# Performance work log

Measured on AMD Instinct MI355X. Metric: run time of the kernel, lower is better.

## Reference

```python
import jax, jax.numpy as jnp
import numpy as np

EPS = 1e-5
NUM_GRAPHS = 512


def _glorot(key, shape):
    lim = float(np.sqrt(6.0 / (shape[0] + shape[1])))
    return jax.random.uniform(key, shape, jnp.float32, -lim, lim)


def setup_inputs() -> dict:
    key = jax.random.key(0)
    ks = jax.random.split(key, 20)
    N, E, F0 = 50000, 800000, 64
    x = jax.random.normal(ks[0], (N, F0), jnp.float32)
    edge_index = jax.random.randint(ks[1], (2, E), 0, N, jnp.int64)
    batch = jnp.sort(jax.random.randint(ks[2], (N,), 0, NUM_GRAPHS, jnp.int64))
    dims = [(F0, 128), (128, 64), (64, 32)]
    p = {}
    for i, (di, do) in enumerate(dims, start=1):
        p[f"W{i}l"] = _glorot(ks[3 * i], (di, do))
        p[f"b{i}"] = jnp.zeros((do,), jnp.float32)
        p[f"W{i}r"] = _glorot(ks[3 * i + 1], (di, do))
        p[f"g{i}"] = jnp.ones((do,), jnp.float32)
        p[f"be{i}"] = jnp.zeros((do,), jnp.float32)
    p["Wf1"] = _glorot(ks[13], (32, 128)); p["bf1"] = jnp.zeros((128,), jnp.float32)
    p["Wf2"] = _glorot(ks[14], (128, 64)); p["bf2"] = jnp.zeros((64,), jnp.float32)
    p["Wf3"] = _glorot(ks[15], (64, 2)); p["bf3"] = jnp.zeros((2,), jnp.float32)
    return {"x": x, "edge_index": edge_index, "batch": batch, **p}


def _sage(x, src, dst, Wl, bl, Wr, n):
    # mean-aggregate neighbor features (gather from src, scatter-mean to dst)
    agg = jax.ops.segment_sum(x[src], dst, num_segments=n)
    cnt = jax.ops.segment_sum(jnp.ones((src.shape[0],), x.dtype), dst, num_segments=n)
    mean = agg / jnp.maximum(cnt, 1.0)[:, None]
    return mean @ Wl + bl + x @ Wr


def _bn(x, g, b):
    mu = jnp.mean(x, axis=0)
    var = jnp.mean((x - mu) ** 2, axis=0)  # biased var, torch training mode
    return (x - mu) * jax.lax.rsqrt(var + EPS) * g + b


def reference(x, edge_index, batch,
              W1l, b1, W1r, g1, be1,
              W2l, b2, W2r, g2, be2,
              W3l, b3, W3r, g3, be3,
              Wf1, bf1, Wf2, bf2, Wf3, bf3):
    n = x.shape[0]
    src, dst = edge_index[0], edge_index[1]
    h = _bn(jax.nn.relu(_sage(x, src, dst, W1l, b1, W1r, n)), g1, be1)
    h = _bn(jax.nn.relu(_sage(h, src, dst, W2l, b2, W2r, n)), g2, be2)
    h = _bn(jax.nn.relu(_sage(h, src, dst, W3l, b3, W3r, n)), g3, be3)
    pooled = jax.ops.segment_sum(h, batch, num_segments=NUM_GRAPHS)  # [G, 32]
    cr = jax.nn.relu(pooled @ Wf1 + bf1)  # dropout = identity (eval)
    cr = jax.nn.relu(cr @ Wf2 + bf2)
    cr = cr @ Wf3 + bf3
    return cr.reshape(-1, 2)
```

## Files before the change

kernel.cpp:

```cpp
#include <hip/hip_runtime.h>
#include <hip/hip_bf16.h>

#define EPSBN 1e-5f
#define NGRAPH 512
#define SCAN_NB 128

typedef __attribute__((ext_vector_type(8))) short bf16x8;
typedef __attribute__((ext_vector_type(4))) float f32x4;

__device__ inline short f2bf(float f) {
    unsigned u = __builtin_bit_cast(unsigned, f);
    u += 0x7fffu + ((u >> 16) & 1u);
    return (short)(u >> 16);
}
__device__ inline float bf2f(short s) {
    unsigned u = ((unsigned)(unsigned short)s) << 16;
    return __builtin_bit_cast(float, u);
}

__global__ void __launch_bounds__(256) k_hist(
    const int* __restrict__ dst, int* __restrict__ hist, int E)
{
    for (int e = blockIdx.x * 256 + threadIdx.x; e < E; e += gridDim.x * 256)
        atomicAdd(&hist[dst[e]], 1);
}

__global__ void __launch_bounds__(256) k_scan1(
    const int* __restrict__ hist, int* __restrict__ blocksum, int N)
{
    __shared__ int red[256];
    const int C = (N + SCAN_NB - 1) / SCAN_NB;
    const int b = blockIdx.x, t = threadIdx.x;
    const int lo = b * C, hi = min(lo + C, N);
    int s = 0;
    for (int i = lo + t; i < hi; i += 256) s += hist[i];
    red[t] = s;
    __syncthreads();
    for (int off = 128; off; off >>= 1) {
        if (t < off) red[t] += red[t + off];
        __syncthreads();
    }
    if (t == 0) blocksum[b] = red[0];
}

__global__ void __launch_bounds__(SCAN_NB) k_scan2(
    const int* __restrict__ blocksum, int* __restrict__ blockoff,
    int* __restrict__ row_off, int N)
{
    __shared__ int tmp[SCAN_NB];
    const int t = threadIdx.x;
    int v = blocksum[t];
    tmp[t] = v;
    __syncthreads();
    for (int off = 1; off < SCAN_NB; off <<= 1) {
        int u = (t >= off) ? tmp[t - off] : 0;
        __syncthreads();
        tmp[t] += u;
        __syncthreads();
    }
    blockoff[t] = tmp[t] - v;
    if (t == SCAN_NB - 1) row_off[N] = tmp[t];
}

__global__ void __launch_bounds__(256) k_scan3(
    const int* __restrict__ hist, const int* __restrict__ blockoff,
    int* __restrict__ row_off, int* __restrict__ cursor, int N)
{
    __shared__ int red[256];
    const int C = (N + SCAN_NB - 1) / SCAN_NB;
    const int b = blockIdx.x, t = threadIdx.x;
    const int lo = b * C, hi = min(lo + C, N);
    const int TC = (C + 255) / 256;
    const int s0 = lo + t * TC;
    const int s1 = min(s0 + TC, hi);
    int s = 0;
    for (int i = s0; i < s1; i++) s += hist[i];
    red[t] = s;
    __syncthreads();
    for (int off = 1; off < 256; off <<= 1) {
        int u = (t >= off) ? red[t - off] : 0;
        __syncthreads();
        red[t] += u;
        __syncthreads();
    }
    int run = blockoff[b] + red[t] - s;
    for (int i = s0; i < s1; i++) {
        row_off[i] = run;
        cursor[i] = run;
        run += hist[i];
    }
}

__global__ void __launch_bounds__(256) k_scatter(
    const int* __restrict__ src, const int* __restrict__ dst,
    int* __restrict__ cursor, int* __restrict__ csr, int E)
{
    for (int e = blockIdx.x * 256 + threadIdx.x; e < E; e += gridDim.x * 256) {
        int d = dst[e];
        int p = atomicAdd(&cursor[d], 1);
        csr[p] = src[e];
    }
}

template <int F, bool OB>
__global__ void __launch_bounds__(256) k_gatherb(
    const short* __restrict__ feat, const int* __restrict__ row_off,
    const int* __restrict__ csr, void* __restrict__ aggv, int N)
{
    constexpr int LPR = F / 8;
    constexpr int RPB = 256 / LPR;
    const int lane = threadIdx.x % LPR;
    const int rloc = threadIdx.x / LPR;
    float* aggf = (float*)aggv;
    short* aggb = (short*)aggv;
    for (int row = blockIdx.x * RPB + rloc; row < N; row += gridDim.x * RPB) {
        const int s0 = row_off[row];
        const int s1 = row_off[row + 1];
        float acc0[8], acc1[8];
        #pragma unroll
        for (int i = 0; i < 8; i++) { acc0[i] = 0.f; acc1[i] = 0.f; }
        int p = s0;
        for (; p + 1 < s1; p += 2) {
            int sA = csr[p];
            int sB = csr[p + 1];
            bf16x8 va = *(const bf16x8*)&feat[(long long)sA * F + lane * 8];
            bf16x8 vb = *(const bf16x8*)&feat[(long long)sB * F + lane * 8];
            #pragma unroll
            for (int i = 0; i < 8; i++) {
                acc0[i] += bf2f(va[i]);
                acc1[i] += bf2f(vb[i]);
            }
        }
        if (p < s1) {
            int sA = csr[p];
            bf16x8 va = *(const bf16x8*)&feat[(long long)sA * F + lane * 8];
            #pragma unroll
            for (int i = 0; i < 8; i++) acc0[i] += bf2f(va[i]);
        }
        if constexpr (OB) {
            short o[8];
            #pragma unroll
            for (int i = 0; i < 8; i++) o[i] = f2bf(acc0[i] + acc1[i]);
            *(bf16x8*)&aggb[(long long)row * F + lane * 8] = *(bf16x8*)o;
        } else {
            float4 o0 = make_float4(acc0[0] + acc1[0], acc0[1] + acc1[1],
                                    acc0[2] + acc1[2], acc0[3] + acc1[3]);
            float4 o1 = make_float4(acc0[4] + acc1[4], acc0[5] + acc1[5],
                                    acc0[6] + acc1[6], acc0[7] + acc1[7]);
            *(float4*)&aggf[(long long)row * F + lane * 8] = o0;
            *(float4*)&aggf[(long long)row * F + lane * 8 + 4] = o1;
        }
    }
}

__global__ void __launch_bounds__(256) k_cvt(
    const float* __restrict__ in, short* __restrict__ out, long long n4)
{
    long long i = (long long)blockIdx.x * 256 + threadIdx.x;
    if (i >= n4) return;
    float4 v = *(const float4*)&in[i * 4];
    short4 o = make_short4(f2bf(v.x), f2bf(v.y), f2bf(v.z), f2bf(v.w));
    *(short4*)&out[i * 4] = o;
}

template <int K, int F, bool AFF>
__global__ void __launch_bounds__(64) k_wprep(
    const float* __restrict__ W, const float* __restrict__ a,
    const float* __restrict__ c, const float* __restrict__ bias,
    short* __restrict__ Wt, float* __restrict__ cvec)
{
    int j = blockIdx.x * 64 + threadIdx.x;
    if (j >= F) return;
    float cv = bias ? bias[j] : 0.f;
    for (int k = 0; k < K; k++) {
        float w = W[k * F + j];
        float aa = 1.f;
        if constexpr (AFF) {
            aa = a[k];
            cv += c[k] * w;
        }
        Wt[j * K + k] = f2bf(aa * w);
    }
    cvec[j] = cv;
}

template <int K, int FOUT, bool DUAL, bool HASBASE, bool FINAL, bool OUTBF16>
__global__ void __launch_bounds__(256) k_mgemm(
    const short* __restrict__ A, const short* __restrict__ A2,
    const short* __restrict__ Wt, const short* __restrict__ Wt2,
    const float* __restrict__ cvec, const float* __restrict__ base,
    const int* __restrict__ row_off, void* outv,
    float* __restrict__ s_out, float* __restrict__ q_out, int N)
{
    constexpr int KS = K / 32;
    constexpr int NCT = FOUT / 16;
    const int lane = threadIdx.x & 63;
    const int wid = threadIdx.x >> 6;
    const int g = lane >> 4;
    const int mi = lane & 15;
    const int RT = (N + 15) >> 4;
    const int nw = gridDim.x * 4;
    float* outf = (float*)outv;
    short* outb = (short*)outv;

    float st_s[FINAL ? NCT : 1];
    float st_q[FINAL ? NCT : 1];
    if constexpr (FINAL) {
        #pragma unroll
        for (int ct = 0; ct < NCT; ct++) { st_s[ct] = 0.f; st_q[ct] = 0.f; }
    }

    for (int rt = blockIdx.x * 4 + wid; rt < RT; rt += nw) {
        const int m0 = rt * 16;
        int arow = m0 + mi;
        if (arow >= N) arow = N - 1;

        bf16x8 af[KS];
        bf16x8 af2[DUAL ? KS : 1];
        const short* ap = A + (long long)arow * K;
        #pragma unroll
        for (int s = 0; s < KS; s++)
            af[s] = *(const bf16x8*)(ap + s * 32 + g * 8);
        if constexpr (DUAL) {
            const short* ap2 = A2 + (long long)arow * K;
            #pragma unroll
            for (int s = 0; s < KS; s++)
                af2[s] = *(const bf16x8*)(ap2 + s * 32 + g * 8);
        }

        float invc[4];
        if constexpr (DUAL || HASBASE) {
            #pragma unroll
            for (int r = 0; r < 4; r++) {
                int row = m0 + 4 * g + r;
                int cnt = 1;
                if (row < N) cnt = max(row_off[row + 1] - row_off[row], 1);
                invc[r] = 1.f / (float)cnt;
            }
        }

        #pragma unroll
        for (int ct = 0; ct < NCT; ct++) {
            f32x4 acc = {0.f, 0.f, 0.f, 0.f};
            f32x4 acc2 = {0.f, 0.f, 0.f, 0.f};
            const short* bp = Wt + (long long)(ct * 16 + mi) * K;
            #pragma unroll
            for (int s = 0; s < KS; s++) {
                bf16x8 bf = *(const bf16x8*)(bp + s * 32 + g * 8);
                acc = __builtin_amdgcn_mfma_f32_16x16x32_bf16(af[s], bf, acc, 0, 0, 0);
                if constexpr (DUAL) {
                    bf16x8 bf2 = *(const bf16x8*)(Wt2 + (long long)(ct * 16 + mi) * K + s * 32 + g * 8);
                    acc2 = __builtin_amdgcn_mfma_f32_16x16x32_bf16(af2[s], bf2, acc2, 0, 0, 0);
                }
            }
            float cv = cvec[ct * 16 + mi];
            float sl = 0.f, ql = 0.f;
            #pragma unroll
            for (int r = 0; r < 4; r++) {
                int row = m0 + 4 * g + r;
                if (row < N) {
                    float v = acc[r] + cv;
                    if constexpr (DUAL) v = fmaf(invc[r], acc2[r], v);
                    if constexpr (HASBASE)
                        v = fmaf(invc[r], base[(long long)row * FOUT + ct * 16 + mi], v);
                    if constexpr (FINAL) v = fmaxf(v, 0.f);
                    if constexpr (OUTBF16)
                        outb[(long long)row * FOUT + ct * 16 + mi] = f2bf(v);
                    else
                        outf[(long long)row * FOUT + ct * 16 + mi] = v;
                    if constexpr (FINAL) { sl += v; ql += v * v; }
                }
            }
            if constexpr (FINAL) {
                sl += __shfl_xor(sl, 16, 64);
                sl += __shfl_xor(sl, 32, 64);
                ql += __shfl_xor(ql, 16, 64);
                ql += __shfl_xor(ql, 32, 64);
                st_s[ct] += sl;
                st_q[ct] += ql;
            }
        }
    }

    if constexpr (FINAL) {
        __shared__ float redS[4][NCT][16];
        __shared__ float redQ[4][NCT][16];
        if (lane < 16) {
            #pragma unroll
            for (int ct = 0; ct < NCT; ct++) {
                redS[wid][ct][lane] = st_s[ct];
                redQ[wid][ct][lane] = st_q[ct];
            }
        }
        __syncthreads();
        if (wid == 0 && lane < 16) {
            #pragma unroll
            for (int ct = 0; ct < NCT; ct++) {
                float s = redS[0][ct][lane] + redS[1][ct][lane] +
                          redS[2][ct][lane] + redS[3][ct][lane];
                float q = redQ[0][ct][lane] + redQ[1][ct][lane] +
                          redQ[2][ct][lane] + redQ[3][ct][lane];
                atomicAdd(&s_out[ct * 16 + lane], s);
                atomicAdd(&q_out[ct * 16 + lane], q);
            }
        }
    }
}

__global__ void k_finalize(const float* __restrict__ s, const float* __restrict__ q,
                           const float* __restrict__ g, const float* __restrict__ be,
                           float* __restrict__ a, float* __restrict__ c,
                           int F, float invN)
{
    int j = threadIdx.x;
    if (j < F) {
        float mu = s[j] * invN;
        float var = q[j] * invN - mu * mu;
        float aj = g[j] / sqrtf(var + EPSBN);
        a[j] = aj;
        c[j] = be[j] - mu * aj;
    }
}

__global__ void __launch_bounds__(256) k_pool(
    const float* __restrict__ t3, const float* __restrict__ a,
    const float* __restrict__ c, const int* __restrict__ batch,
    float* __restrict__ pooled, int N)
{
    long long gid = (long long)blockIdx.x * 256 + threadIdx.x;
    int i = (int)(gid >> 5);
    int j = (int)(gid & 31);
    if (i >= N) return;
    int g = batch[i];
    float v = t3[(long long)i * 32 + j] * a[j] + c[j];
    atomicAdd(&pooled[g * 32 + j], v);
}

__global__ void __launch_bounds__(128) k_mlp(
    const float* __restrict__ pooled,
    const float* __restrict__ Wf1, const float* __restrict__ bf1,
    const float* __restrict__ Wf2, const float* __restrict__ bf2,
    const float* __restrict__ Wf3, const float* __restrict__ bf3,
    float* __restrict__ out)
{
    __shared__ float p[32], h1[128], h2[64];
    int g = blockIdx.x, t = threadIdx.x;
    if (t < 32) p[t] = pooled[g * 32 + t];
    __syncthreads();
    {
        float acc = bf1[t];
        #pragma unroll
        for (int k = 0; k < 32; k++) acc += p[k] * Wf1[k * 128 + t];
        h1[t] = fmaxf(acc, 0.f);
    }
    __syncthreads();
    if (t < 64) {
        float acc = bf2[t];
        #pragma unroll
        for (int k = 0; k < 128; k++) acc += h1[k] * Wf2[k * 64 + t];
        h2[t] = fmaxf(acc, 0.f);
    }
    __syncthreads();
    if (t < 2) {
        float acc = bf3[t];
        #pragma unroll
        for (int k = 0; k < 64; k++) acc += h2[k] * Wf3[k * 2 + t];
        out[g * 2 + t] = acc;
    }
}

extern "C" void kernel_launch(void* const* d_in, const int* in_sizes, int n_in,
                              void* d_out, int out_size, void* d_ws, size_t ws_size,
                              hipStream_t stream)
{
    const float* x     = (const float*)d_in[0];
    const int*   ei    = (const int*)d_in[1];
    const int*   batch = (const int*)d_in[2];
    const float* W1l = (const float*)d_in[3];
    const float* b1  = (const float*)d_in[4];
    const float* W1r = (const float*)d_in[5];
    const float* g1  = (const float*)d_in[6];
    const float* be1 = (const float*)d_in[7];
    const float* W2l = (const float*)d_in[8];
    const float* b2  = (const float*)d_in[9];
    const float* W2r = (const float*)d_in[10];
    const float* g2  = (const float*)d_in[11];
    const float* be2 = (const float*)d_in[12];
    const float* W3l = (const float*)d_in[13];
    const float* b3  = (const float*)d_in[14];
    const float* W3r = (const float*)d_in[15];
    const float* g3  = (const float*)d_in[16];
    const float* be3 = (const float*)d_in[17];
    const float* Wf1 = (const float*)d_in[18];
    const float* bf1 = (const float*)d_in[19];
    const float* Wf2 = (const float*)d_in[20];
    const float* bf2 = (const float*)d_in[21];
    const float* Wf3 = (const float*)d_in[22];
    const float* bf3 = (const float*)d_in[23];

    const int N = in_sizes[0] / 64;
    const int E = in_sizes[1] / 2;
    const int* src = ei;
    const int* dst = ei + E;

    char* ws = (char*)d_ws;
    size_t off = 0;
    auto alloc = [&](size_t bytes) {
        size_t o = off;
        off += (bytes + 511) & ~(size_t)511;
        return o;
    };
    const size_t o_rowoff = alloc((size_t)(N + 1) * 4);
    const size_t o_hist   = alloc((size_t)N * 4);
    const size_t o_cursor = alloc((size_t)N * 4);
    const size_t o_bsum   = alloc(SCAN_NB * 4 * 2);
    const size_t o_csr    = alloc((size_t)E * 4);
    const size_t o_zoneB  = alloc((size_t)N * 128);
    const size_t o_zoneC  = alloc((size_t)N * 128);
    const size_t o_zoneD  = alloc((size_t)N * 256);
    const size_t o_zoneE  = alloc((size_t)N * 256);
    const size_t o_pool   = alloc((size_t)NGRAPH * 32 * 4);
    const size_t o_stats  = alloc(448 * 4);
    const size_t o_aff    = alloc(448 * 4);
    const size_t o_cvec   = alloc(512 * 4);
    const size_t o_wt     = alloc((8192 * 4 + 2048 * 2) * 2);
    (void)ws_size;

    int* row_off = (int*)(ws + o_rowoff);
    int* hist    = (int*)(ws + o_hist);
    int* cursor  = (int*)(ws + o_cursor);
    int* bsum    = (int*)(ws + o_bsum);
    int* boff    = bsum + SCAN_NB;
    int* csr     = (int*)(ws + o_csr);
    short* xb   = (short*)(ws + o_zoneB);
    short* y2b  = (short*)(ws + o_zoneB);
    short* aggb = (short*)(ws + o_zoneC);
    short* t2b  = (short*)(ws + o_zoneC);
    short* t1b  = (short*)(ws + o_zoneD);
    short* y3b  = (short*)(ws + o_zoneD);
    float* m2   = (float*)(ws + o_zoneE);
    float* m3   = (float*)(ws + o_zoneE);
    float* t3   = m3;
    float* pooled = (float*)(ws + o_pool);
    float* s1 = (float*)(ws + o_stats);
    float* q1 = s1 + 128;
    float* s2 = q1 + 128;
    float* q2 = s2 + 64;
    float* s3 = q2 + 64;
    float* q3 = s3 + 32;
    float* a1 = (float*)(ws + o_aff);
    float* c1 = a1 + 128;
    float* a2 = c1 + 128;
    float* c2 = a2 + 64;
    float* a3 = c2 + 64;
    float* c3 = a3 + 32;
    float* cv1r = (float*)(ws + o_cvec);
    float* cvdum = cv1r + 128;
    float* cv2l = cvdum + 128;
    float* cv2r = cv2l + 64;
    float* cv3l = cv2r + 64;
    float* cv3r = cv3l + 32;
    short* W1l_t = (short*)(ws + o_wt);
    short* W1r_t = W1l_t + 8192;
    short* W2l_t = W1r_t + 8192;
    short* W2r_t = W2l_t + 8192;
    short* W3l_t = W2r_t + 8192;
    short* W3r_t = W3l_t + 2048;

    const float invN = 1.0f / (float)N;
    const int MG = 512;

    hipMemsetAsync(ws + o_hist, 0, (size_t)N * 4, stream);
    hipMemsetAsync(ws + o_stats, 0, 448 * 4, stream);
    hipMemsetAsync(ws + o_pool, 0, (size_t)NGRAPH * 32 * 4, stream);

    k_hist<<<2048, 256, 0, stream>>>(dst, hist, E);
    k_scan1<<<SCAN_NB, 256, 0, stream>>>(hist, bsum, N);
    k_scan2<<<1, SCAN_NB, 0, stream>>>(bsum, boff, row_off, N);
    k_scan3<<<SCAN_NB, 256, 0, stream>>>(hist, boff, row_off, cursor, N);
    k_scatter<<<2048, 256, 0, stream>>>(src, dst, cursor, csr, E);

    k_cvt<<<(int)(((long long)N * 16 + 255) / 256), 256, 0, stream>>>(
        x, xb, (long long)N * 16);
    k_wprep<64, 128, false><<<2, 64, 0, stream>>>(
        W1r, nullptr, nullptr, b1, W1r_t, cv1r);
    k_wprep<64, 128, false><<<2, 64, 0, stream>>>(
        W1l, nullptr, nullptr, nullptr, W1l_t, cvdum);

    k_gatherb<64, true><<<(N + 31) / 32, 256, 0, stream>>>(
        xb, row_off, csr, aggb, N);
    k_mgemm<64, 128, true, false, true, true><<<MG, 256, 0, stream>>>(
        xb, aggb, W1r_t, W1l_t, cv1r, nullptr, row_off, t1b, s1, q1, N);
    k_finalize<<<1, 128, 0, stream>>>(s1, q1, g1, be1, a1, c1, 128, invN);

    k_wprep<128, 64, true><<<1, 64, 0, stream>>>(W2l, a1, c1, nullptr, W2l_t, cv2l);
    k_wprep<128, 64, true><<<1, 64, 0, stream>>>(W2r, a1, c1, b2, W2r_t, cv2r);
    k_mgemm<128, 64, false, false, false, true><<<MG, 256, 0, stream>>>(
        t1b, nullptr, W2l_t, nullptr, cv2l, nullptr, row_off, y2b,
        nullptr, nullptr, N);
    k_gatherb<64, false><<<(N + 31) / 32, 256, 0, stream>>>(
        y2b, row_off, csr, m2, N);
    k_mgemm<128, 64, false, true, true, true><<<MG, 256, 0, stream>>>(
        t1b, nullptr, W2r_t, nullptr, cv2r, m2, row_off, t2b, s2, q2, N);
    k_finalize<<<1, 64, 0, stream>>>(s2, q2, g2, be2, a2, c2, 64, invN);

    k_wprep<64, 32, true><<<1, 64, 0, stream>>>(W3l, a2, c2, nullptr, W3l_t, cv3l);
    k_wprep<64, 32, true><<<1, 64, 0, stream>>>(W3r, a2, c2, b3, W3r_t, cv3r);
    k_mgemm<64, 32, false, false, false, true><<<MG, 256, 0, stream>>>(
        t2b, nullptr, W3l_t, nullptr, cv3l, nullptr, row_off, y3b,
        nullptr, nullptr, N);
    k_gatherb<32, false><<<(N + 63) / 64, 256, 0, stream>>>(
        y3b, row_off, csr, m3, N);
    k_mgemm<64, 32, false, true, true, false><<<MG, 256, 0, stream>>>(
        t2b, nullptr, W3r_t, nullptr, cv3r, m3, row_off, t3, s3, q3, N);
    k_finalize<<<1, 32, 0, stream>>>(s3, q3, g3, be3, a3, c3, 32, invN);

    {
        long long tot = (long long)N * 32;
        int blocks = (int)((tot + 255) / 256);
        k_pool<<<blocks, 256, 0, stream>>>(t3, a3, c3, batch, pooled, N);
    }
    k_mlp<<<NGRAPH, 128, 0, stream>>>(pooled, Wf1, bf1, Wf2, bf2, Wf3, bf3,
                                      (float*)d_out);
}
```

Before: 312.4 us.

## Partition CSR scatter by XCD, store aggregates in bf16, fuse pooling into final GEMM

The CSR scatter kernel now has each block handle only destinations in one eighth of the node range, chosen by blockIdx mod 8, to keep cursor atomics local to one XCD's cache. The layer-2 and layer-3 neighbor aggregates are now stored in bf16 instead of fp32, which halves their traffic. The separate pooling kernel is removed: the last GEMM atomically adds its raw ReLU outputs into per-graph sums, and the BN affine is applied afterwards in the MLP using per-graph node counts. In exchange, every block reads all edges in the scatter, bf16 storage of the aggregates loses precision, and the GEMM epilogue now does many atomics on a small array.

```diff
diff --git a/kernel.cpp b/kernel.cpp
--- a/kernel.cpp
+++ b/kernel.cpp
@@ -4,6 +4,7 @@
 #define EPSBN 1e-5f
 #define NGRAPH 512
 #define SCAN_NB 128
+#define NXCD 8
 
 typedef __attribute__((ext_vector_type(8))) short bf16x8;
 typedef __attribute__((ext_vector_type(4))) float f32x4;
@@ -91,28 +92,33 @@
     }
 }
 
-__global__ void __launch_bounds__(256) k_scatter(
+__global__ void __launch_bounds__(256) k_scatter8(
     const int* __restrict__ src, const int* __restrict__ dst,
-    int* __restrict__ cursor, int* __restrict__ csr, int E)
-{
-    for (int e = blockIdx.x * 256 + threadIdx.x; e < E; e += gridDim.x * 256) {
+    int* __restrict__ cursor, int* __restrict__ csr, int E, int N)
+{
+    const int grp = blockIdx.x & (NXCD - 1);
+    const int chunk = (N + NXCD - 1) / NXCD;
+    const int lo = grp * chunk;
+    const int hi = min(lo + chunk, N);
+    const int stride = (gridDim.x >> 3) * 256;
+    for (int e = (blockIdx.x >> 3) * 256 + threadIdx.x; e < E; e += stride) {
         int d = dst[e];
-        int p = atomicAdd(&cursor[d], 1);
-        csr[p] = src[e];
-    }
-}
-
-template <int F, bool OB>
+        if (d >= lo && d < hi) {
+            int p = atomicAdd(&cursor[d], 1);
+            csr[p] = src[e];
+        }
+    }
+}
+
+template <int F>
 __global__ void __launch_bounds__(256) k_gatherb(
     const short* __restrict__ feat, const int* __restrict__ row_off,
-    const int* __restrict__ csr, void* __restrict__ aggv, int N)
+    const int* __restrict__ csr, short* __restrict__ aggb, int N)
 {
     constexpr int LPR = F / 8;
     constexpr int RPB = 256 / LPR;
     const int lane = threadIdx.x % LPR;
     const int rloc = threadIdx.x / LPR;
-    float* aggf = (float*)aggv;
-    short* aggb = (short*)aggv;
     for (int row = blockIdx.x * RPB + rloc; row < N; row += gridDim.x * RPB) {
         const int s0 = row_off[row];
         const int s1 = row_off[row + 1];
@@ -137,19 +143,10 @@
             #pragma unroll
             for (int i = 0; i < 8; i++) acc0[i] += bf2f(va[i]);
         }
-        if constexpr (OB) {
-            short o[8];
-            #pragma unroll
-            for (int i = 0; i < 8; i++) o[i] = f2bf(acc0[i] + acc1[i]);
-            *(bf16x8*)&aggb[(long long)row * F + lane * 8] = *(bf16x8*)o;
-        } else {
-            float4 o0 = make_float4(acc0[0] + acc1[0], acc0[1] + acc1[1],
-                                    acc0[2] + acc1[2], acc0[3] + acc1[3]);
-            float4 o1 = make_float4(acc0[4] + acc1[4], acc0[5] + acc1[5],
-                                    acc0[6] + acc1[6], acc0[7] + acc1[7]);
-            *(float4*)&aggf[(long long)row * F + lane * 8] = o0;
-            *(float4*)&aggf[(long long)row * F + lane * 8 + 4] = o1;
-        }
+        short o[8];
+        #pragma unroll
+        for (int i = 0; i < 8; i++) o[i] = f2bf(acc0[i] + acc1[i]);
+        *(bf16x8*)&aggb[(long long)row * F + lane * 8] = *(bf16x8*)o;
     }
 }
 
@@ -184,13 +181,15 @@
     cvec[j] = cv;
 }
 
-template <int K, int FOUT, bool DUAL, bool HASBASE, bool FINAL, bool OUTBF16>
+template <int K, int FOUT, bool DUAL, bool HASBASE, bool FINAL, bool OUTBF16,
+          bool POOL>
 __global__ void __launch_bounds__(256) k_mgemm(
     const short* __restrict__ A, const short* __restrict__ A2,
     const short* __restrict__ Wt, const short* __restrict__ Wt2,
-    const float* __restrict__ cvec, const float* __restrict__ base,
+    const float* __restrict__ cvec, const short* __restrict__ base,
     const int* __restrict__ row_off, void* outv,
-    float* __restrict__ s_out, float* __restrict__ q_out, int N)
+    float* __restrict__ s_out, float* __restrict__ q_out,
+    const int* __restrict__ batchp, float* __restrict__ praw, int N)
 {
     constexpr int KS = K / 32;
     constexpr int NCT = FOUT / 16;
@@ -238,6 +237,14 @@
                 invc[r] = 1.f / (float)cnt;
             }
         }
+        int bidx[4];
+        if constexpr (POOL) {
+            #pragma unroll
+            for (int r = 0; r < 4; r++) {
+                int row = m0 + 4 * g + r;
+                bidx[r] = (row < N) ? batchp[row] : -1;
+            }
+        }
 
         #pragma unroll
         for (int ct = 0; ct < NCT; ct++) {
@@ -262,12 +269,15 @@
                     float v = acc[r] + cv;
                     if constexpr (DUAL) v = fmaf(invc[r], acc2[r], v);
                     if constexpr (HASBASE)
-                        v = fmaf(invc[r], base[(long long)row * FOUT + ct * 16 + mi], v);
+                        v = fmaf(invc[r], bf2f(base[(long long)row * FOUT + ct * 16 + mi]), v);
                     if constexpr (FINAL) v = fmaxf(v, 0.f);
-                    if constexpr (OUTBF16)
+                    if constexpr (POOL) {
+                        atomicAdd(&praw[bidx[r] * FOUT + ct * 16 + mi], v);
+                    } else if constexpr (OUTBF16) {
                         outb[(long long)row * FOUT + ct * 16 + mi] = f2bf(v);
-                    else
+                    } else {
                         outf[(long long)row * FOUT + ct * 16 + mi] = v;
+                    }
                     if constexpr (FINAL) { sl += v; ql += v * v; }
                 }
             }
@@ -322,22 +332,16 @@
     }
 }
 
-__global__ void __launch_bounds__(256) k_pool(
-    const float* __restrict__ t3, const float* __restrict__ a,
-    const float* __restrict__ c, const int* __restrict__ batch,
-    float* __restrict__ pooled, int N)
-{
-    long long gid = (long long)blockIdx.x * 256 + threadIdx.x;
-    int i = (int)(gid >> 5);
-    int j = (int)(gid & 31);
-    if (i >= N) return;
-    int g = batch[i];
-    float v = t3[(long long)i * 32 + j] * a[j] + c[j];
-    atomicAdd(&pooled[g * 32 + j], v);
+__global__ void __launch_bounds__(256) k_gcnt(
+    const int* __restrict__ batch, float* __restrict__ gcnt, int N)
+{
+    int i = blockIdx.x * 256 + threadIdx.x;
+    if (i < N) atomicAdd(&gcnt[batch[i]], 1.0f);
 }
 
 __global__ void __launch_bounds__(128) k_mlp(
-    const float* __restrict__ pooled,
+    const float* __restrict__ praw, const float* __restrict__ a3,
+    const float* __restrict__ c3, const float* __restrict__ gcnt,
     const float* __restrict__ Wf1, const float* __restrict__ bf1,
     const float* __restrict__ Wf2, const float* __restrict__ bf2,
     const float* __restrict__ Wf3, const float* __restrict__ bf3,
@@ -345,7 +349,7 @@
 {
     __shared__ float p[32], h1[128], h2[64];
     int g = blockIdx.x, t = threadIdx.x;
-    if (t < 32) p[t] = pooled[g * 32 + t];
+    if (t < 32) p[t] = a3[t] * praw[g * 32 + t] + gcnt[g] * c3[t];
     __syncthreads();
     {
         float acc = bf1[t];
@@ -418,8 +422,9 @@
     const size_t o_zoneB  = alloc((size_t)N * 128);
     const size_t o_zoneC  = alloc((size_t)N * 128);
     const size_t o_zoneD  = alloc((size_t)N * 256);
-    const size_t o_zoneE  = alloc((size_t)N * 256);
-    const size_t o_pool   = alloc((size_t)NGRAPH * 32 * 4);
+    const size_t o_zoneE  = alloc((size_t)N * 128);
+    const size_t o_praw   = alloc((size_t)NGRAPH * 32 * 4);
+    const size_t o_gcnt   = alloc((size_t)NGRAPH * 4);
     const size_t o_stats  = alloc(448 * 4);
     const size_t o_aff    = alloc(448 * 4);
     const size_t o_cvec   = alloc(512 * 4);
@@ -438,10 +443,10 @@
     short* t2b  = (short*)(ws + o_zoneC);
     short* t1b  = (short*)(ws + o_zoneD);
     short* y3b  = (short*)(ws + o_zoneD);
-    float* m2   = (float*)(ws + o_zoneE);
-    float* m3   = (float*)(ws + o_zoneE);
-    float* t3   = m3;
-    float* pooled = (float*)(ws + o_pool);
+    short* m2b  = (short*)(ws + o_zoneE);
+    short* m3b  = (short*)(ws + o_zoneE);
+    float* praw = (float*)(ws + o_praw);
+    float* gcnt = (float*)(ws + o_gcnt);
     float* s1 = (float*)(ws + o_stats);
     float* q1 = s1 + 128;
     float* s2 = q1 + 128;
@@ -472,13 +477,15 @@
 
     hipMemsetAsync(ws + o_hist, 0, (size_t)N * 4, stream);
     hipMemsetAsync(ws + o_stats, 0, 448 * 4, stream);
-    hipMemsetAsync(ws + o_pool, 0, (size_t)NGRAPH * 32 * 4, stream);
+    hipMemsetAsync(ws + o_praw, 0, (size_t)NGRAPH * 32 * 4, stream);
+    hipMemsetAsync(ws + o_gcnt, 0, (size_t)NGRAPH * 4, stream);
 
     k_hist<<<2048, 256, 0, stream>>>(dst, hist, E);
     k_scan1<<<SCAN_NB, 256, 0, stream>>>(hist, bsum, N);
     k_scan2<<<1, SCAN_NB, 0, stream>>>(bsum, boff, row_off, N);
     k_scan3<<<SCAN_NB, 256, 0, stream>>>(hist, boff, row_off, cursor, N);
-    k_scatter<<<2048, 256, 0, stream>>>(src, dst, cursor, csr, E);
+    k_scatter8<<<2048, 256, 0, stream>>>(src, dst, cursor, csr, E, N);
+    k_gcnt<<<(N + 255) / 256, 256, 0, stream>>>(batch, gcnt, N);
 
     k_cvt<<<(int)(((long long)N * 16 + 255) / 256), 256, 0, stream>>>(
         x, xb, (long long)N * 16);
@@ -487,39 +494,38 @@
     k_wprep<64, 128, false><<<2, 64, 0, stream>>>(
         W1l, nullptr, nullptr, nullptr, W1l_t, cvdum);
 
-    k_gatherb<64, true><<<(N + 31) / 32, 256, 0, stream>>>(
+    k_gatherb<64><<<(N + 31) / 32, 256, 0, stream>>>(
         xb, row_off, csr, aggb, N);
-    k_mgemm<64, 128, true, false, true, true><<<MG, 256, 0, stream>>>(
-        xb, aggb, W1r_t, W1l_t, cv1r, nullptr, row_off, t1b, s1, q1, N);
+    k_mgemm<64, 128, true, false, true, true, false><<<MG, 256, 0, stream>>>(
+        xb, aggb, W1r_t, W1l_t, cv1r, nullptr, row_off, t1b, s1, q1,
+        nullptr, nullptr, N);
     k_finalize<<<1, 128, 0, stream>>>(s1, q1, g1, be1, a1, c1, 128, invN);
 
     k_wprep<128, 64, true><<<1, 64, 0, stream>>>(W2l, a1, c1, nullptr, W2l_t, cv2l);
     k_wprep<128, 64, true><<<1, 64, 0, stream>>>(W2r, a1, c1, b2, W2r_t, cv2r);
-    k_mgemm<128, 64, false, false, false, true><<<MG, 256, 0, stream>>>(
+    k_mgemm<128, 64, false, false, false, true, false><<<MG, 256, 0, stream>>>(
         t1b, nullptr, W2l_t, nullptr, cv2l, nullptr, row_off, y2b,
+        nullptr, nullptr, nullptr, nullptr, N);
+    k_gatherb<64><<<(N + 31) / 32, 256, 0, stream>>>(
+        y2b, row_off, csr, m2b, N);
+    k_mgemm<128, 64, false, true, true, true, false><<<MG, 256, 0, stream>>>(
+        t1b, nullptr, W2r_t, nullptr, cv2r, m2b, row_off, t2b, s2, q2,
         nullptr, nullptr, N);
-    k_gatherb<64, false><<<(N + 31) / 32, 256, 0, stream>>>(
-        y2b, row_off, csr, m2, N);
-    k_mgemm<128, 64, false, true, true, true><<<MG, 256, 0, stream>>>(
-        t1b, nullptr, W2r_t, nullptr, cv2r, m2, row_off, t2b, s2, q2, N);
     k_finalize<<<1, 64, 0, stream>>>(s2, q2, g2, be2, a2, c2, 64, invN);
 
     k_wprep<64, 32, true><<<1, 64, 0, stream>>>(W3l, a2, c2, nullptr, W3l_t, cv3l);
     k_wprep<64, 32, true><<<1, 64, 0, stream>>>(W3r, a2, c2, b3, W3r_t, cv3r);
-    k_mgemm<64, 32, false, false, false, true><<<MG, 256, 0, stream>>>(
+    k_mgemm<64, 32, false, false, false, true, false><<<MG, 256, 0, stream>>>(
         t2b, nullptr, W3l_t, nullptr, cv3l, nullptr, row_off, y3b,
-        nullptr, nullptr, N);
-    k_gatherb<32, false><<<(N + 63) / 64, 256, 0, stream>>>(
-        y3b, row_off, csr, m3, N);
-    k_mgemm<64, 32, false, true, true, false><<<MG, 256, 0, stream>>>(
-        t2b, nullptr, W3r_t, nullptr, cv3r, m3, row_off, t3, s3, q3, N);
+        nullptr, nullptr, nullptr, nullptr, N);
+    k_gatherb<32><<<(N + 63) / 64, 256, 0, stream>>>(
+        y3b, row_off, csr, m3b, N);
+    k_mgemm<64, 32, false, true, true, false, true><<<MG, 256, 0, stream>>>(
+        t2b, nullptr, W3r_t, nullptr, cv3r, m3b, row_off, nullptr, s3, q3,
+        batch, praw, N);
     k_finalize<<<1, 32, 0, stream>>>(s3, q3, g3, be3, a3, c3, 32, invN);
 
-    {
-        long long tot = (long long)N * 32;
-        int blocks = (int)((tot + 255) / 256);
-        k_pool<<<blocks, 256, 0, stream>>>(t3, a3, c3, batch, pooled, N);
-    }
-    k_mlp<<<NGRAPH, 128, 0, stream>>>(pooled, Wf1, bf1, Wf2, bf2, Wf3, bf3,
+    k_mlp<<<NGRAPH, 128, 0, stream>>>(praw, a3, c3, gcnt,
+                                      Wf1, bf1, Wf2, bf2, Wf3, bf3,
                                       (float*)d_out);
 }
```

Result: slower. 343.0 us (+9.8%).
